# Optimization experiments

Measured on AMD Instinct MI355X. Metric: run time of the kernel, lower is better.

## Reference

```python
import jax, jax.numpy as jnp
import numpy as np

H = 2048
D = 66
T = 4096

def _lstm_cell(x, h, c, W_ih, W_hh, b_ih, b_hh):
    # x: [1, in], h/c: [1, H]; torch LSTMCell gate order: i, f, g, o
    gates = x @ W_ih.T + h @ W_hh.T + b_ih + b_hh  # [1, 4H]
    i, f, g, o = jnp.split(gates, 4, axis=-1)
    i = jax.nn.sigmoid(i)
    f = jax.nn.sigmoid(f)
    g = jnp.tanh(g)
    o = jax.nn.sigmoid(o)
    c_new = f * c + i * g
    h_new = o * jnp.tanh(c_new)
    return h_new, c_new

def setup_inputs() -> dict:
    key = jax.random.key(0)
    ks = jax.random.split(key, 12)
    s1 = 1.0 / np.sqrt(H)
    mk = lambda k, shp: jax.random.uniform(k, shp, jnp.float32, -s1, s1)
    return {
        "y": jax.random.normal(ks[0], (T, D), jnp.float32),
        "W_ih1": mk(ks[1], (4 * H, D)),
        "W_hh1": mk(ks[2], (4 * H, H)),
        "b_ih1": mk(ks[3], (4 * H,)),
        "b_hh1": mk(ks[4], (4 * H,)),
        "W_ih2": mk(ks[5], (4 * H, H)),
        "W_hh2": mk(ks[6], (4 * H, H)),
        "b_ih2": mk(ks[7], (4 * H,)),
        "b_hh2": mk(ks[8], (4 * H,)),
        "W_lin": mk(ks[9], (D, H)),
        "b_lin": mk(ks[10], (D,)),
        "pre_output_len": 64,
    }

def reference(y, W_ih1, W_hh1, b_ih1, b_hh1, W_ih2, W_hh2, b_ih2, b_hh2, W_lin, b_lin, pre_output_len):
    frames = y[:, None, :]  # [T, 1, D]

    def step(carry, x):
        h1, c1, h2, c2 = carry
        h1, c1 = _lstm_cell(x, h1, c1, W_ih1, W_hh1, b_ih1, b_hh1)
        h2, c2 = _lstm_cell(h1, h2, c2, W_ih2, W_hh2, b_ih2, b_hh2)
        out = h2 @ W_lin.T + b_lin  # [1, D]
        return (h1, c1, h2, c2), out

    z = jnp.zeros((1, H), jnp.float32)
    _, outs = jax.lax.scan(step, (z, z, z, z), frames)  # [T, 1, D]
    return outs[pre_output_len:]
```

## Files before the change

### kernel.cpp

```cpp
#include <hip/hip_runtime.h>
#include <math.h>

#define HH 2048
#define DD 66
#define TT 4096
#define PRE 64
#define NWG 256
#define RPW 8
#define FSTRIDE 16


__device__ __forceinline__ float sigmoidf_(float x) {
  return 1.0f / (1.0f + expf(-x));
}

__device__ __forceinline__ void gbar_wait(unsigned* flags, unsigned target, int tid) {
  unsigned v = __hip_atomic_load(&flags[tid * FSTRIDE], __ATOMIC_RELAXED, __HIP_MEMORY_SCOPE_AGENT);
  while (!__syncthreads_and((int)(v == target))) {
    v = __hip_atomic_load(&flags[tid * FSTRIDE], __ATOMIC_RELAXED, __HIP_MEMORY_SCOPE_AGENT);
  }
}

__global__ __launch_bounds__(256, 1) void lstm_persist(
    const float* __restrict__ y,
    const float* __restrict__ Wih1, const float* __restrict__ Whh1,
    const float* __restrict__ bih1, const float* __restrict__ bhh1,
    const float* __restrict__ Wih2, const float* __restrict__ Whh2,
    const float* __restrict__ bih2, const float* __restrict__ bhh2,
    const float* __restrict__ Wlin, const float* __restrict__ blin,
    float* __restrict__ out,
    float* h1buf, float* h2buf, unsigned* flags1, unsigned* flags2)
{
  __shared__ __align__(16) float ldsH1[HH];
  __shared__ __align__(16) float ldsH2[HH];
  __shared__ float ldsX[DD];
  __shared__ float g1s[4][RPW];
  __shared__ float g2s[4][RPW];
  __shared__ float c1s[RPW];
  __shared__ float c2s[RPW];
  __shared__ float red[4];

  const int tid  = threadIdx.x;
  const int wg   = blockIdx.x;
  const int wave = tid >> 6;
  const int lane = tid & 63;
  const int rowbase = wg * RPW;
  const int grow0   = wave * HH + rowbase;

  for (int i = tid; i < HH; i += 256) { ldsH1[i] = 0.0f; ldsH2[i] = 0.0f; }
  if (tid < RPW) {
    c1s[tid] = 0.0f; c2s[tid] = 0.0f;
    __hip_atomic_store(&h2buf[HH + rowbase + tid], 0.0f, __ATOMIC_RELAXED, __HIP_MEMORY_SCOPE_AGENT);
  }
  __syncthreads();

  for (int t = 0; t < TT; ++t) {
    if (tid < DD) ldsX[tid] = y[t * DD + tid];
    __syncthreads();

    {
      float4 acc[RPW];
      #pragma unroll
      for (int r = 0; r < RPW; ++r) acc[r] = make_float4(0.f, 0.f, 0.f, 0.f);
      const float4* h4 = (const float4*)ldsH1;
      #pragma unroll 2
      for (int j = 0; j < 8; ++j) {
        const float4 hv = h4[j * 64 + lane];
        #pragma unroll
        for (int r = 0; r < RPW; ++r) {
          const float4* Wr = (const float4*)(Whh1 + (size_t)(grow0 + r) * HH);
          float4 wv = Wr[j * 64 + lane];
          acc[r].x = fmaf(wv.x, hv.x, acc[r].x);
          acc[r].y = fmaf(wv.y, hv.y, acc[r].y);
          acc[r].z = fmaf(wv.z, hv.z, acc[r].z);
          acc[r].w = fmaf(wv.w, hv.w, acc[r].w);
        }
      }
      #pragma unroll
      for (int r = 0; r < RPW; ++r) {
        const int grow = grow0 + r;
        float a = (acc[r].x + acc[r].y) + (acc[r].z + acc[r].w);
        const float* Xr = Wih1 + (size_t)grow * DD;
        a += Xr[lane] * ldsX[lane];
        if (lane < DD - 64) a += Xr[64 + lane] * ldsX[64 + lane];
        #pragma unroll
        for (int s = 32; s > 0; s >>= 1) a += __shfl_xor(a, s, 64);
        if (lane == 0) g1s[wave][r] = a + bih1[grow] + bhh1[grow];
      }
    }
    __syncthreads();

    if (tid < RPW) {
      float gi = sigmoidf_(g1s[0][tid]);
      float gf = sigmoidf_(g1s[1][tid]);
      float gg = tanhf(g1s[2][tid]);
      float go = sigmoidf_(g1s[3][tid]);
      float c  = fmaf(gf, c1s[tid], gi * gg);
      c1s[tid] = c;
      float h  = go * tanhf(c);
      __hip_atomic_store(&h1buf[(t & 1) * HH + rowbase + tid], h,
                         __ATOMIC_RELAXED, __HIP_MEMORY_SCOPE_AGENT);
    }
    __syncthreads();
    if (tid == 0)
      __hip_atomic_store(&flags1[wg * FSTRIDE], (unsigned)(t + 1),
                         __ATOMIC_RELEASE, __HIP_MEMORY_SCOPE_AGENT);
    gbar_wait(flags1, (unsigned)(t + 1), tid);

    for (int i = tid; i < HH; i += 256) {
      ldsH1[i] = __hip_atomic_load(&h1buf[(t & 1) * HH + i],
                                   __ATOMIC_RELAXED, __HIP_MEMORY_SCOPE_AGENT);
      ldsH2[i] = __hip_atomic_load(&h2buf[((t + 1) & 1) * HH + i],
                                   __ATOMIC_RELAXED, __HIP_MEMORY_SCOPE_AGENT);
    }
    __syncthreads();

    {
      float4 acc[RPW];
      #pragma unroll
      for (int r = 0; r < RPW; ++r) acc[r] = make_float4(0.f, 0.f, 0.f, 0.f);
      const float4* ha = (const float4*)ldsH1;
      const float4* hb = (const float4*)ldsH2;
      #pragma unroll 2
      for (int j = 0; j < 8; ++j) {
        const float4 va = ha[j * 64 + lane];
        const float4 vb = hb[j * 64 + lane];
        #pragma unroll
        for (int r = 0; r < RPW; ++r) {
          const float4* Wa = (const float4*)(Wih2 + (size_t)(grow0 + r) * HH);
          const float4* Wb = (const float4*)(Whh2 + (size_t)(grow0 + r) * HH);
          float4 wa = Wa[j * 64 + lane];
          float4 wb = Wb[j * 64 + lane];
          acc[r].x = fmaf(wa.x, va.x, acc[r].x);
          acc[r].y = fmaf(wa.y, va.y, acc[r].y);
          acc[r].z = fmaf(wa.z, va.z, acc[r].z);
          acc[r].w = fmaf(wa.w, va.w, acc[r].w);
          acc[r].x = fmaf(wb.x, vb.x, acc[r].x);
          acc[r].y = fmaf(wb.y, vb.y, acc[r].y);
          acc[r].z = fmaf(wb.z, vb.z, acc[r].z);
          acc[r].w = fmaf(wb.w, vb.w, acc[r].w);
        }
      }
      #pragma unroll
      for (int r = 0; r < RPW; ++r) {
        const int grow = grow0 + r;
        float a = (acc[r].x + acc[r].y) + (acc[r].z + acc[r].w);
        #pragma unroll
        for (int s = 32; s > 0; s >>= 1) a += __shfl_xor(a, s, 64);
        if (lane == 0) g2s[wave][r] = a + bih2[grow] + bhh2[grow];
      }
    }
    __syncthreads();

    if (tid < RPW) {
      float gi = sigmoidf_(g2s[0][tid]);
      float gf = sigmoidf_(g2s[1][tid]);
      float gg = tanhf(g2s[2][tid]);
      float go = sigmoidf_(g2s[3][tid]);
      float c  = fmaf(gf, c2s[tid], gi * gg);
      c2s[tid] = c;
      float h  = go * tanhf(c);
      __hip_atomic_store(&h2buf[(t & 1) * HH + rowbase + tid], h,
                         __ATOMIC_RELAXED, __HIP_MEMORY_SCOPE_AGENT);
    }
    __syncthreads();
    if (tid == 0)
      __hip_atomic_store(&flags2[wg * FSTRIDE], (unsigned)(t + 1),
                         __ATOMIC_RELEASE, __HIP_MEMORY_SCOPE_AGENT);

    if (wg < DD && t >= PRE + 1) {
      const float4* Wr = (const float4*)(Wlin + (size_t)wg * HH);
      const float4* h4 = (const float4*)ldsH2;
      float p = 0.f;
      #pragma unroll
      for (int j = 0; j < 2; ++j) {
        int idx = tid + j * 256;
        float4 wv = Wr[idx]; float4 hv = h4[idx];
        p += wv.x * hv.x + wv.y * hv.y + wv.z * hv.z + wv.w * hv.w;
      }
      #pragma unroll
      for (int s = 32; s > 0; s >>= 1) p += __shfl_xor(p, s, 64);
      if (lane == 0) red[wave] = p;
      __syncthreads();
      if (tid == 0)
        out[(size_t)(t - 1 - PRE) * DD + wg] = red[0] + red[1] + red[2] + red[3] + blin[wg];
    }

    gbar_wait(flags2, (unsigned)(t + 1), tid);
  }

  if (wg < DD) {
    for (int i = tid; i < HH; i += 256)
      ldsH2[i] = __hip_atomic_load(&h2buf[((TT - 1) & 1) * HH + i],
                                   __ATOMIC_RELAXED, __HIP_MEMORY_SCOPE_AGENT);
    __syncthreads();
    const float4* Wr = (const float4*)(Wlin + (size_t)wg * HH);
    const float4* h4 = (const float4*)ldsH2;
    float p = 0.f;
    #pragma unroll
    for (int j = 0; j < 2; ++j) {
      int idx = tid + j * 256;
      float4 wv = Wr[idx]; float4 hv = h4[idx];
      p += wv.x * hv.x + wv.y * hv.y + wv.z * hv.z + wv.w * hv.w;
    }
    #pragma unroll
    for (int s = 32; s > 0; s >>= 1) p += __shfl_xor(p, s, 64);
    if (lane == 0) red[wave] = p;
    __syncthreads();
    if (tid == 0)
      out[(size_t)(TT - 1 - PRE) * DD + wg] = red[0] + red[1] + red[2] + red[3] + blin[wg];
  }
}

extern "C" void kernel_launch(void* const* d_in, const int* in_sizes, int n_in,
                              void* d_out, int out_size, void* d_ws, size_t ws_size,
                              hipStream_t stream) {
  const float* y    = (const float*)d_in[0];
  const float* Wih1 = (const float*)d_in[1];
  const float* Whh1 = (const float*)d_in[2];
  const float* bih1 = (const float*)d_in[3];
  const float* bhh1 = (const float*)d_in[4];
  const float* Wih2 = (const float*)d_in[5];
  const float* Whh2 = (const float*)d_in[6];
  const float* bih2 = (const float*)d_in[7];
  const float* bhh2 = (const float*)d_in[8];
  const float* Wlin = (const float*)d_in[9];
  const float* blin = (const float*)d_in[10];
  float* out = (float*)d_out;

  char* ws = (char*)d_ws;
  float*    h1buf  = (float*)(ws);
  float*    h2buf  = (float*)(ws + 2 * HH * sizeof(float));
  unsigned* flags1 = (unsigned*)(ws + 4 * HH * sizeof(float));
  unsigned* flags2 = flags1 + NWG * FSTRIDE;

  void* args[] = { &y, &Wih1, &Whh1, &bih1, &bhh1, &Wih2, &Whh2, &bih2, &bhh2,
                   &Wlin, &blin, &out, &h1buf, &h2buf, &flags1, &flags2 };
  hipLaunchCooperativeKernel((const void*)lstm_persist, dim3(NWG), dim3(256),
                             args, 0, stream);
}
```

Measured before the change: 202.4 ms.

## Keep split fp16+int8 LSTM weights resident on-chip and overlap layer barriers

Rewrites the persistent LSTM kernel so that all three recurrent weight matrices are loaded once. Each weight is split into an fp16 high part plus an int8 residual and kept in registers and LDS, which removes the per-step streaming of weights from HBM/L2. Hidden states are exchanged as fp16 hi/lo pairs and accumulated with packed fdot2. The layer-2 recurrent pass is moved ahead of the layer-1 barrier wait to overlap synchronisation, and the output projection uses atomicAdd across waves. It adds quantization error, heavy register and LDS pressure, and an abort-timeout path in the barrier. Correctness also depends on the output buffer being zeroed, since results are now accumulated with atomicAdd.

```diff
diff --git a/kernel.cpp b/kernel.cpp
--- a/kernel.cpp
+++ b/kernel.cpp
@@ -9,19 +9,149 @@
 #define RPW 8
 #define FSTRIDE 16
 
-
-__device__ __forceinline__ float sigmoidf_(float x) {
-  return 1.0f / (1.0f + expf(-x));
-}
-
-__device__ __forceinline__ void gbar_wait(unsigned* flags, unsigned target, int tid) {
-  unsigned v = __hip_atomic_load(&flags[tid * FSTRIDE], __ATOMIC_RELAXED, __HIP_MEMORY_SCOPE_AGENT);
-  while (!__syncthreads_and((int)(v == target))) {
-    v = __hip_atomic_load(&flags[tid * FSTRIDE], __ATOMIC_RELAXED, __HIP_MEMORY_SCOPE_AGENT);
-  }
-}
-
-__global__ __launch_bounds__(256, 1) void lstm_persist(
+#define S_HI 0.015625f
+#define S_LO 7.62939453125e-06f
+#define S_RS (1.0f / 16646144.0f)
+#define RQ   260096.0f
+#define F16_MIN_NORM 6.104e-05f
+
+typedef _Float16 f16x2 __attribute__((ext_vector_type(2)));
+
+#if defined(__HIP_DEVICE_COMPILE__) && __has_builtin(__builtin_amdgcn_fdot2)
+#define FDOT2(a, b, c) __builtin_amdgcn_fdot2((a), (b), (c), false)
+#else
+#define FDOT2(a, b, c) fmaf((float)(a).y, (float)(b).y, fmaf((float)(a).x, (float)(b).x, (c)))
+#endif
+
+__device__ __forceinline__ f16x2 u2h(unsigned u) { return __builtin_bit_cast(f16x2, u); }
+
+__device__ __forceinline__ void unp8(unsigned u, f16x2& plo, f16x2& phi) {
+  unsigned t0 = (u & 0x000000FFu) | ((u << 8) & 0x00FF0000u);
+  unsigned t1 = ((u >> 16) & 0x000000FFu) | ((u >> 8) & 0x00FF0000u);
+  t0 = (t0 ^ 0x00800080u) | 0x64006400u;
+  t1 = (t1 ^ 0x00800080u) | 0x64006400u;
+  f16x2 K; K.x = (_Float16)1152.0f; K.y = (_Float16)1152.0f;
+  plo = u2h(t0) - K;
+  phi = u2h(t1) - K;
+}
+
+__device__ __forceinline__ int q8(float x) {
+  float s = x * RQ;
+  s = fminf(fmaxf(s, -127.0f), 127.0f);
+  return (int)rintf(s);
+}
+
+__device__ __forceinline__ unsigned splitw(float2 f, f16x2* hi) {
+  float a = f.x * 64.0f, b = f.y * 64.0f;
+  _Float16 ha = (_Float16)a, hb = (_Float16)b;
+  float fa = (float)ha, fb = (float)hb;
+  if (fabsf(fa) < F16_MIN_NORM) { ha = (_Float16)0.0f; fa = 0.0f; }
+  if (fabsf(fb) < F16_MIN_NORM) { hb = (_Float16)0.0f; fb = 0.0f; }
+  f16x2 h; h.x = ha; h.y = hb; *hi = h;
+  int qa = q8(a - fa), qb = q8(b - fb);
+  return (unsigned)(qa & 255) | ((unsigned)(qb & 255) << 8);
+}
+
+__device__ __forceinline__ void splith(float h0, float h1, unsigned* uhi, unsigned* ulo) {
+  _Float16 a0 = (_Float16)h0, a1 = (_Float16)h1;
+  float f0 = (float)a0, f1 = (float)a1;
+  if (fabsf(f0) < F16_MIN_NORM) { a0 = (_Float16)0.0f; f0 = 0.0f; }
+  if (fabsf(f1) < F16_MIN_NORM) { a1 = (_Float16)0.0f; f1 = 0.0f; }
+  f16x2 hi; hi.x = a0; hi.y = a1;
+  f16x2 lo; lo.x = (_Float16)((h0 - f0) * 2048.0f); lo.y = (_Float16)((h1 - f1) * 2048.0f);
+  *uhi = __builtin_bit_cast(unsigned, hi);
+  *ulo = __builtin_bit_cast(unsigned, lo);
+}
+
+__device__ __forceinline__ float sigm(float x) { return 1.0f / (1.0f + expf(-x)); }
+
+__device__ __forceinline__ void gbar_wait(unsigned* flags, unsigned* abortw,
+                                          int target, int tid) {
+  int v = (int)__hip_atomic_load(&flags[tid * FSTRIDE], __ATOMIC_RELAXED, __HIP_MEMORY_SCOPE_AGENT);
+  int ab = 0, n = 0;
+  while (!__syncthreads_and((int)((v >= target) | ab))) {
+    v = (int)__hip_atomic_load(&flags[tid * FSTRIDE], __ATOMIC_RELAXED, __HIP_MEMORY_SCOPE_AGENT);
+    if (++n >= (1 << 13)) {
+      if (n >= (1 << 20))
+        __hip_atomic_store(abortw, 1u, __ATOMIC_RELAXED, __HIP_MEMORY_SCOPE_AGENT);
+      ab = (__hip_atomic_load(abortw, __ATOMIC_RELAXED, __HIP_MEMORY_SCOPE_AGENT) == 1u);
+    }
+  }
+}
+
+#define PASS(HBASE, WREG, RESEXPR)                                             \
+  {                                                                            \
+    _Pragma("unroll")                                                          \
+    for (int half = 0; half < 2; ++half) {                                     \
+      unsigned hh[8], hl[8];                                                   \
+      _Pragma("unroll")                                                        \
+      for (int jj = 0; jj < 8; ++jj) {                                         \
+        int p = lane + 64 * (8 * half + jj);                                   \
+        hh[jj] = __hip_atomic_load(&(HBASE)[2 * p],     __ATOMIC_RELAXED, __HIP_MEMORY_SCOPE_AGENT); \
+        hl[jj] = __hip_atomic_load(&(HBASE)[2 * p + 1], __ATOMIC_RELAXED, __HIP_MEMORY_SCOPE_AGENT); \
+      }                                                                        \
+      _Pragma("unroll")                                                        \
+      for (int r = 0; r < RPW; ++r) {                                          \
+        _Pragma("unroll")                                                      \
+        for (int jj = 0; jj < 8; ++jj) {                                       \
+          int j = 8 * half + jj;                                               \
+          accf[r] = FDOT2(WREG[r][j], u2h(hh[jj]), accf[r]);                   \
+          accl[r] = FDOT2(WREG[r][j], u2h(hl[jj]), accl[r]);                   \
+        }                                                                      \
+        _Pragma("unroll")                                                      \
+        for (int kk = 0; kk < 4; ++kk) {                                       \
+          int k = 4 * half + kk;                                               \
+          unsigned u = (RESEXPR);                                              \
+          f16x2 plo, phi; unp8(u, plo, phi);                                   \
+          accr[r] = FDOT2(plo, u2h(hh[2 * kk]),     accr[r]);                  \
+          accr[r] = FDOT2(phi, u2h(hh[2 * kk + 1]), accr[r]);                  \
+        }                                                                      \
+      }                                                                        \
+    }                                                                          \
+  }
+
+#define LOADW(WPTR, WREG, STORE)                                               \
+  {                                                                            \
+    _Pragma("unroll")                                                          \
+    for (int r = 0; r < RPW; ++r) {                                            \
+      const int gro = (r >> 1) * HH + rowbase + 2 * wave + (r & 1);            \
+      const float2* src = (const float2*)((WPTR) + (size_t)gro * HH);          \
+      _Pragma("unroll")                                                        \
+      for (int k = 0; k < 8; ++k) {                                            \
+        float2 f0 = src[lane + 64 * (2 * k)];                                  \
+        float2 f1 = src[lane + 64 * (2 * k + 1)];                              \
+        unsigned b01 = splitw(f0, &WREG[r][2 * k]);                            \
+        unsigned b23 = splitw(f1, &WREG[r][2 * k + 1]);                        \
+        unsigned pk = b01 | (b23 << 16);                                       \
+        STORE;                                                                 \
+      }                                                                        \
+    }                                                                          \
+  }
+
+#define OUTBLK(SLOT, TOUT)                                                     \
+  if (wg < DD) {                                                               \
+    const float2* wrow = (const float2*)(Wlin + (size_t)wg * HH);              \
+    float p = 0.0f;                                                            \
+    _Pragma("unroll")                                                          \
+    for (int i = 0; i < 4; ++i) {                                              \
+      int P = tid + 256 * i;                                                   \
+      unsigned uh = __hip_atomic_load(&h2px[(SLOT) * 2048 + 2 * P],     __ATOMIC_RELAXED, __HIP_MEMORY_SCOPE_AGENT); \
+      unsigned ul = __hip_atomic_load(&h2px[(SLOT) * 2048 + 2 * P + 1], __ATOMIC_RELAXED, __HIP_MEMORY_SCOPE_AGENT); \
+      f16x2 hhv = u2h(uh), hlv = u2h(ul);                                      \
+      float2 wv = wrow[P];                                                     \
+      float hx = fmaf((float)hlv.x, 4.8828125e-4f, (float)hhv.x);              \
+      float hy = fmaf((float)hlv.y, 4.8828125e-4f, (float)hhv.y);              \
+      p = fmaf(wv.x, hx, p); p = fmaf(wv.y, hy, p);                            \
+    }                                                                          \
+    _Pragma("unroll")                                                          \
+    for (int sh = 32; sh > 0; sh >>= 1) p += __shfl_xor(p, sh, 64);            \
+    if (lane == 0) {                                                           \
+      if (wave == 0) p += blin[wg];                                            \
+      atomicAdd(&out[(size_t)(TOUT) * DD + wg], p);                            \
+    }                                                                          \
+  }
+
+__global__ __launch_bounds__(256, 1) void lstm_v5(
     const float* __restrict__ y,
     const float* __restrict__ Wih1, const float* __restrict__ Whh1,
     const float* __restrict__ bih1, const float* __restrict__ bhh1,
@@ -29,187 +159,124 @@
     const float* __restrict__ bih2, const float* __restrict__ bhh2,
     const float* __restrict__ Wlin, const float* __restrict__ blin,
     float* __restrict__ out,
-    float* h1buf, float* h2buf, unsigned* flags1, unsigned* flags2)
+    unsigned* h1px, unsigned* h2px,
+    unsigned* flags1, unsigned* flags2, unsigned* abortw)
 {
-  __shared__ __align__(16) float ldsH1[HH];
-  __shared__ __align__(16) float ldsH2[HH];
-  __shared__ float ldsX[DD];
-  __shared__ float g1s[4][RPW];
-  __shared__ float g2s[4][RPW];
-  __shared__ float c1s[RPW];
-  __shared__ float c2s[RPW];
-  __shared__ float red[4];
-
-  const int tid  = threadIdx.x;
-  const int wg   = blockIdx.x;
+  __shared__ unsigned lds1[16384];
+  __shared__ unsigned ldsb[16384];
+
+  const int tid = threadIdx.x;
+  const int wg = blockIdx.x;
   const int wave = tid >> 6;
   const int lane = tid & 63;
   const int rowbase = wg * RPW;
-  const int grow0   = wave * HH + rowbase;
-
-  for (int i = tid; i < HH; i += 256) { ldsH1[i] = 0.0f; ldsH2[i] = 0.0f; }
-  if (tid < RPW) {
-    c1s[tid] = 0.0f; c2s[tid] = 0.0f;
-    __hip_atomic_store(&h2buf[HH + rowbase + tid], 0.0f, __ATOMIC_RELAXED, __HIP_MEMORY_SCOPE_AGENT);
-  }
+  const int P = wg * 4 + wave;
+
+  f16x2 w1[RPW][16], wa[RPW][16], wb[RPW][16];
+  unsigned wlo2[RPW][8];
+  LOADW(Whh1, w1, (lds1[((wave * RPW + r) * 8 + k) * 64 + lane] = pk))
+  LOADW(Wih2, wa, (wlo2[r][k] = pk))
+  LOADW(Whh2, wb, (ldsb[((wave * RPW + r) * 8 + k) * 64 + lane] = pk))
+
+  float c1v0 = 0.0f, c1v1 = 0.0f, c2v0 = 0.0f, c2v1 = 0.0f;
   __syncthreads();
 
+  #pragma unroll 1
   for (int t = 0; t < TT; ++t) {
-    if (tid < DD) ldsX[tid] = y[t * DD + tid];
-    __syncthreads();
-
-    {
-      float4 acc[RPW];
+    const int cur = t & 1, prv = cur ^ 1;
+
+    float xa = y[(size_t)t * DD + lane];
+    float xb = (lane < DD - 64) ? y[(size_t)t * DD + 64 + lane] : 0.0f;
+    float accf[RPW], accl[RPW], accr[RPW];
+    #pragma unroll
+    for (int r = 0; r < RPW; ++r) { accf[r] = 0.f; accl[r] = 0.f; accr[r] = 0.f; }
+
+    if (t > 0) {
+      PASS((h1px + prv * 2048), w1, lds1[((wave * RPW + r) * 8 + k) * 64 + lane])
+    }
+
+    float gv[RPW];
+    #pragma unroll
+    for (int r = 0; r < RPW; ++r) {
+      const int gro = (r >> 1) * HH + rowbase + 2 * wave + (r & 1);
+      float a = fmaf(accr[r], S_RS, fmaf(accl[r], S_LO, accf[r] * S_HI));
+      a = fmaf(Wih1[(size_t)gro * DD + lane], xa, a);
+      if (lane < DD - 64) a = fmaf(Wih1[(size_t)gro * DD + 64 + lane], xb, a);
       #pragma unroll
-      for (int r = 0; r < RPW; ++r) acc[r] = make_float4(0.f, 0.f, 0.f, 0.f);
-      const float4* h4 = (const float4*)ldsH1;
-      #pragma unroll 2
-      for (int j = 0; j < 8; ++j) {
-        const float4 hv = h4[j * 64 + lane];
-        #pragma unroll
-        for (int r = 0; r < RPW; ++r) {
-          const float4* Wr = (const float4*)(Whh1 + (size_t)(grow0 + r) * HH);
-          float4 wv = Wr[j * 64 + lane];
-          acc[r].x = fmaf(wv.x, hv.x, acc[r].x);
-          acc[r].y = fmaf(wv.y, hv.y, acc[r].y);
-          acc[r].z = fmaf(wv.z, hv.z, acc[r].z);
-          acc[r].w = fmaf(wv.w, hv.w, acc[r].w);
-        }
+      for (int sh = 32; sh > 0; sh >>= 1) a += __shfl_xor(a, sh, 64);
+      gv[r] = a;
+    }
+
+    if (lane == 0) {
+      float hv[2];
+      #pragma unroll
+      for (int q = 0; q < 2; ++q) {
+        const int ro = rowbase + 2 * wave + q;
+        float gi = sigm(gv[q]     + bih1[ro]          + bhh1[ro]);
+        float gf = sigm(gv[2 + q] + bih1[HH + ro]     + bhh1[HH + ro]);
+        float gg = tanhf(gv[4 + q] + bih1[2 * HH + ro] + bhh1[2 * HH + ro]);
+        float go = sigm(gv[6 + q] + bih1[3 * HH + ro] + bhh1[3 * HH + ro]);
+        float cp = (q == 0) ? c1v0 : c1v1;
+        float c = fmaf(gf, cp, gi * gg);
+        if (q == 0) c1v0 = c; else c1v1 = c;
+        hv[q] = go * tanhf(c);
       }
-      #pragma unroll
-      for (int r = 0; r < RPW; ++r) {
-        const int grow = grow0 + r;
-        float a = (acc[r].x + acc[r].y) + (acc[r].z + acc[r].w);
-        const float* Xr = Wih1 + (size_t)grow * DD;
-        a += Xr[lane] * ldsX[lane];
-        if (lane < DD - 64) a += Xr[64 + lane] * ldsX[64 + lane];
-        #pragma unroll
-        for (int s = 32; s > 0; s >>= 1) a += __shfl_xor(a, s, 64);
-        if (lane == 0) g1s[wave][r] = a + bih1[grow] + bhh1[grow];
-      }
-    }
-    __syncthreads();
-
-    if (tid < RPW) {
-      float gi = sigmoidf_(g1s[0][tid]);
-      float gf = sigmoidf_(g1s[1][tid]);
-      float gg = tanhf(g1s[2][tid]);
-      float go = sigmoidf_(g1s[3][tid]);
-      float c  = fmaf(gf, c1s[tid], gi * gg);
-      c1s[tid] = c;
-      float h  = go * tanhf(c);
-      __hip_atomic_store(&h1buf[(t & 1) * HH + rowbase + tid], h,
-                         __ATOMIC_RELAXED, __HIP_MEMORY_SCOPE_AGENT);
+      unsigned uhi, ulo; splith(hv[0], hv[1], &uhi, &ulo);
+      __hip_atomic_store(&h1px[cur * 2048 + 2 * P],     uhi, __ATOMIC_RELAXED, __HIP_MEMORY_SCOPE_AGENT);
+      __hip_atomic_store(&h1px[cur * 2048 + 2 * P + 1], ulo, __ATOMIC_RELAXED, __HIP_MEMORY_SCOPE_AGENT);
     }
     __syncthreads();
     if (tid == 0)
       __hip_atomic_store(&flags1[wg * FSTRIDE], (unsigned)(t + 1),
                          __ATOMIC_RELEASE, __HIP_MEMORY_SCOPE_AGENT);
-    gbar_wait(flags1, (unsigned)(t + 1), tid);
-
-    for (int i = tid; i < HH; i += 256) {
-      ldsH1[i] = __hip_atomic_load(&h1buf[(t & 1) * HH + i],
-                                   __ATOMIC_RELAXED, __HIP_MEMORY_SCOPE_AGENT);
-      ldsH2[i] = __hip_atomic_load(&h2buf[((t + 1) & 1) * HH + i],
-                                   __ATOMIC_RELAXED, __HIP_MEMORY_SCOPE_AGENT);
-    }
-    __syncthreads();
-
-    {
-      float4 acc[RPW];
+
+    #pragma unroll
+    for (int r = 0; r < RPW; ++r) { accf[r] = 0.f; accl[r] = 0.f; accr[r] = 0.f; }
+
+    if (t > 0) {
+      gbar_wait(flags2, abortw, t, tid);
+      PASS((h2px + prv * 2048), wb, ldsb[((wave * RPW + r) * 8 + k) * 64 + lane])
+    }
+
+    gbar_wait(flags1, abortw, t + 1, tid);
+    PASS((h1px + cur * 2048), wa, wlo2[r][k])
+
+    #pragma unroll
+    for (int r = 0; r < RPW; ++r) {
+      float a = fmaf(accr[r], S_RS, fmaf(accl[r], S_LO, accf[r] * S_HI));
       #pragma unroll
-      for (int r = 0; r < RPW; ++r) acc[r] = make_float4(0.f, 0.f, 0.f, 0.f);
-      const float4* ha = (const float4*)ldsH1;
-      const float4* hb = (const float4*)ldsH2;
-      #pragma unroll 2
-      for (int j = 0; j < 8; ++j) {
-        const float4 va = ha[j * 64 + lane];
-        const float4 vb = hb[j * 64 + lane];
-        #pragma unroll
-        for (int r = 0; r < RPW; ++r) {
-          const float4* Wa = (const float4*)(Wih2 + (size_t)(grow0 + r) * HH);
-          const float4* Wb = (const float4*)(Whh2 + (size_t)(grow0 + r) * HH);
-          float4 wa = Wa[j * 64 + lane];
-          float4 wb = Wb[j * 64 + lane];
-          acc[r].x = fmaf(wa.x, va.x, acc[r].x);
-          acc[r].y = fmaf(wa.y, va.y, acc[r].y);
-          acc[r].z = fmaf(wa.z, va.z, acc[r].z);
-          acc[r].w = fmaf(wa.w, va.w, acc[r].w);
-          acc[r].x = fmaf(wb.x, vb.x, acc[r].x);
-          acc[r].y = fmaf(wb.y, vb.y, acc[r].y);
-          acc[r].z = fmaf(wb.z, vb.z, acc[r].z);
-          acc[r].w = fmaf(wb.w, vb.w, acc[r].w);
-        }
+      for (int sh = 32; sh > 0; sh >>= 1) a += __shfl_xor(a, sh, 64);
+      gv[r] = a;
+    }
+
+    if (lane == 0) {
+      float hv[2];
+      #pragma unroll
+      for (int q = 0; q < 2; ++q) {
+        const int ro = rowbase + 2 * wave + q;
+        float gi = sigm(gv[q]     + bih2[ro]          + bhh2[ro]);
+        float gf = sigm(gv[2 + q] + bih2[HH + ro]     + bhh2[HH + ro]);
+        float gg = tanhf(gv[4 + q] + bih2[2 * HH + ro] + bhh2[2 * HH + ro]);
+        float go = sigm(gv[6 + q] + bih2[3 * HH + ro] + bhh2[3 * HH + ro]);
+        float cp = (q == 0) ? c2v0 : c2v1;
+        float c = fmaf(gf, cp, gi * gg);
+        if (q == 0) c2v0 = c; else c2v1 = c;
+        hv[q] = go * tanhf(c);
       }
-      #pragma unroll
-      for (int r = 0; r < RPW; ++r) {
-        const int grow = grow0 + r;
-        float a = (acc[r].x + acc[r].y) + (acc[r].z + acc[r].w);
-        #pragma unroll
-        for (int s = 32; s > 0; s >>= 1) a += __shfl_xor(a, s, 64);
-        if (lane == 0) g2s[wave][r] = a + bih2[grow] + bhh2[grow];
-      }
-    }
-    __syncthreads();
-
-    if (tid < RPW) {
-      float gi = sigmoidf_(g2s[0][tid]);
-      float gf = sigmoidf_(g2s[1][tid]);
-      float gg = tanhf(g2s[2][tid]);
-      float go = sigmoidf_(g2s[3][tid]);
-      float c  = fmaf(gf, c2s[tid], gi * gg);
-      c2s[tid] = c;
-      float h  = go * tanhf(c);
-      __hip_atomic_store(&h2buf[(t & 1) * HH + rowbase + tid], h,
-                         __ATOMIC_RELAXED, __HIP_MEMORY_SCOPE_AGENT);
+      unsigned uhi, ulo; splith(hv[0], hv[1], &uhi, &ulo);
+      __hip_atomic_store(&h2px[cur * 2048 + 2 * P],     uhi, __ATOMIC_RELAXED, __HIP_MEMORY_SCOPE_AGENT);
+      __hip_atomic_store(&h2px[cur * 2048 + 2 * P + 1], ulo, __ATOMIC_RELAXED, __HIP_MEMORY_SCOPE_AGENT);
     }
     __syncthreads();
     if (tid == 0)
       __hip_atomic_store(&flags2[wg * FSTRIDE], (unsigned)(t + 1),
                          __ATOMIC_RELEASE, __HIP_MEMORY_SCOPE_AGENT);
 
-    if (wg < DD && t >= PRE + 1) {
-      const float4* Wr = (const float4*)(Wlin + (size_t)wg * HH);
-      const float4* h4 = (const float4*)ldsH2;
-      float p = 0.f;
-      #pragma unroll
-      for (int j = 0; j < 2; ++j) {
-        int idx = tid + j * 256;
-        float4 wv = Wr[idx]; float4 hv = h4[idx];
-        p += wv.x * hv.x + wv.y * hv.y + wv.z * hv.z + wv.w * hv.w;
-      }
-      #pragma unroll
-      for (int s = 32; s > 0; s >>= 1) p += __shfl_xor(p, s, 64);
-      if (lane == 0) red[wave] = p;
-      __syncthreads();
-      if (tid == 0)
-        out[(size_t)(t - 1 - PRE) * DD + wg] = red[0] + red[1] + red[2] + red[3] + blin[wg];
-    }
-
-    gbar_wait(flags2, (unsigned)(t + 1), tid);
-  }
-
-  if (wg < DD) {
-    for (int i = tid; i < HH; i += 256)
-      ldsH2[i] = __hip_atomic_load(&h2buf[((TT - 1) & 1) * HH + i],
-                                   __ATOMIC_RELAXED, __HIP_MEMORY_SCOPE_AGENT);
-    __syncthreads();
-    const float4* Wr = (const float4*)(Wlin + (size_t)wg * HH);
-    const float4* h4 = (const float4*)ldsH2;
-    float p = 0.f;
-    #pragma unroll
-    for (int j = 0; j < 2; ++j) {
-      int idx = tid + j * 256;
-      float4 wv = Wr[idx]; float4 hv = h4[idx];
-      p += wv.x * hv.x + wv.y * hv.y + wv.z * hv.z + wv.w * hv.w;
-    }
-    #pragma unroll
-    for (int s = 32; s > 0; s >>= 1) p += __shfl_xor(p, s, 64);
-    if (lane == 0) red[wave] = p;
-    __syncthreads();
-    if (tid == 0)
-      out[(size_t)(TT - 1 - PRE) * DD + wg] = red[0] + red[1] + red[2] + red[3] + blin[wg];
-  }
+    if (t >= PRE + 1) { OUTBLK(prv, t - 1 - PRE) }
+  }
+
+  gbar_wait(flags2, abortw, TT, tid);
+  { OUTBLK(((TT - 1) & 1), TT - 1 - PRE) }
 }
 
 extern "C" void kernel_launch(void* const* d_in, const int* in_sizes, int n_in,
@@ -228,14 +295,20 @@
   const float* blin = (const float*)d_in[10];
   float* out = (float*)d_out;
 
-  char* ws = (char*)d_ws;
-  float*    h1buf  = (float*)(ws);
-  float*    h2buf  = (float*)(ws + 2 * HH * sizeof(float));
-  unsigned* flags1 = (unsigned*)(ws + 4 * HH * sizeof(float));
+  unsigned* ws = (unsigned*)d_ws;
+  unsigned* h1px   = ws;
+  unsigned* h2px   = h1px + 4096;
+  unsigned* flags1 = h2px + 4096;
   unsigned* flags2 = flags1 + NWG * FSTRIDE;
+  unsigned* abortw = flags2 + NWG * FSTRIDE;
 
   void* args[] = { &y, &Wih1, &Whh1, &bih1, &bhh1, &Wih2, &Whh2, &bih2, &bhh2,
-                   &Wlin, &blin, &out, &h1buf, &h2buf, &flags1, &flags2 };
-  hipLaunchCooperativeKernel((const void*)lstm_persist, dim3(NWG), dim3(256),
-                             args, 0, stream);
-}
+                   &Wlin, &blin, &out, &h1px, &h2px, &flags1, &flags2, &abortw };
+  hipError_t e = hipLaunchCooperativeKernel((const void*)lstm_v5, dim3(NWG),
+                                            dim3(256), args, 0, stream);
+  if (e != hipSuccess) {
+    hipLaunchKernelGGL(lstm_v5, dim3(NWG), dim3(256), 0, stream,
+                       y, Wih1, Whh1, bih1, bhh1, Wih2, Whh2, bih2, bhh2,
+                       Wlin, blin, out, h1px, h2px, flags1, flags2, abortw);
+  }
+}
```

Measured after the change: 276.6 ms. 36.7% more time.
